# Kernel tuning notes

Hardware: AMD Instinct MI355X
Metric: run time of the kernel (lower is better)

The kernel has to match this reference:

```python
import jax, jax.numpy as jnp
import numpy as np

B, S, D, H = 2, 2048, 1024, 16
DH = D // H  # 64
EPS = 1e-5


def setup_inputs() -> dict:
    key = jax.random.key(0)
    ks = jax.random.split(key, 16)
    s = 0.02
    return {
        "emb": jax.random.normal(ks[0], (B, S, D), dtype=jnp.float32),
        # per-head projections, stacked: torch Linear weight layout [out, in] -> [H, DH, D]
        "Wq": jax.random.normal(ks[1], (H, DH, D), dtype=jnp.float32) * s,
        "bq": jnp.zeros((H, DH), dtype=jnp.float32),
        "Wk": jax.random.normal(ks[2], (H, DH, D), dtype=jnp.float32) * s,
        "bk": jnp.zeros((H, DH), dtype=jnp.float32),
        "Wv": jax.random.normal(ks[3], (H, DH, D), dtype=jnp.float32) * s,
        "bv": jnp.zeros((H, DH), dtype=jnp.float32),
        "W0": jax.random.normal(ks[4], (D, D), dtype=jnp.float32) * s,
        "b0": jnp.zeros((D,), dtype=jnp.float32),
        "g1": jnp.ones((D,), dtype=jnp.float32),
        "be1": jnp.zeros((D,), dtype=jnp.float32),
        "W1": jax.random.normal(ks[5], (4 * D, D), dtype=jnp.float32) * s,
        "b1": jnp.zeros((4 * D,), dtype=jnp.float32),
        "W2": jax.random.normal(ks[6], (D, 4 * D), dtype=jnp.float32) * s,
        "b2": jnp.zeros((D,), dtype=jnp.float32),
        "g2": jnp.ones((D,), dtype=jnp.float32),
        "be2": jnp.zeros((D,), dtype=jnp.float32),
    }


def _layer_norm(x, g, b):
    mu = jnp.mean(x, axis=-1, keepdims=True)
    var = jnp.mean(jnp.square(x - mu), axis=-1, keepdims=True)
    return (x - mu) * jax.lax.rsqrt(var + EPS) * g + b


def reference(emb, Wq, bq, Wk, bk, Wv, bv, W0, b0, g1, be1, W1, b1, W2, b2, g2, be2):
    # per-head Q/K/V projections, batched over heads  -> [B, H, S, DH]
    q = jnp.einsum("bsd,hed->bhse", emb, Wq) + bq[None, :, None, :]
    k = jnp.einsum("bsd,hed->bhse", emb, Wk) + bk[None, :, None, :]
    v = jnp.einsum("bsd,hed->bhse", emb, Wv) + bv[None, :, None, :]
    # NOTE: original module applies NO scale before softmax; it divides the
    # softmax(QK^T) @ V output by sqrt(d_head) afterwards. Kept faithfully.
    scores = jnp.einsum("bhse,bhte->bhst", q, k)  # [B,H,S,S]
    attn = jax.nn.softmax(scores, axis=-1)
    z = jnp.einsum("bhst,bhte->bhse", attn, v) / np.sqrt(DH).astype(np.float32)
    # concat heads along feature dim (head 0 first) -> [B, S, D]
    z = z.transpose(0, 2, 1, 3).reshape(B, S, D)
    z = z @ W0.T + b0
    out1 = _layer_norm(z + emb, g1, be1)
    h = jax.nn.relu(out1 @ W1.T + b1)  # [B, S, 4D]
    out2 = _layer_norm(out1 + (h @ W2.T + b2), g2, be2)
    return out2
```

## Files before the change

### kernel.cpp

```cpp
#include <hip/hip_runtime.h>
#include <hip/hip_bf16.h>
#include <cstdint>
#include <cmath>

#define DEV __device__ __forceinline__

typedef float f32x4 __attribute__((ext_vector_type(4)));
typedef float f32x16 __attribute__((ext_vector_type(16)));
typedef __bf16 bf16x8 __attribute__((ext_vector_type(8)));
typedef unsigned short u16;
typedef u16 u16x8 __attribute__((ext_vector_type(8)));
typedef u16 u16x4 __attribute__((ext_vector_type(4)));

DEV u16 f2bf(float f) {
  union { float f; uint32_t u; } x{f};
  uint32_t r = x.u + 0x7FFFu + ((x.u >> 16) & 1u);
  return (u16)(r >> 16);
}

DEV void gl_lds16(const u16* g, u16* l) {
  __builtin_amdgcn_global_load_lds((const __attribute__((address_space(1))) void*)g,
                                   (__attribute__((address_space(3))) void*)l, 16, 0, 0);
}

__global__ __launch_bounds__(256) void k_cvt(const float* __restrict__ s,
                                             u16* __restrict__ d, int n) {
  int step = gridDim.x * blockDim.x * 4;
  for (int i = (blockIdx.x * blockDim.x + threadIdx.x) * 4; i < n; i += step) {
    float4 v = *reinterpret_cast<const float4*>(s + i);
    u16x4 o;
    o[0] = f2bf(v.x); o[1] = f2bf(v.y); o[2] = f2bf(v.z); o[3] = f2bf(v.w);
    *reinterpret_cast<u16x4*>(d + i) = o;
  }
}

__global__ __launch_bounds__(256) void k_cvt4(
    const float* __restrict__ s0, const float* __restrict__ s1,
    const float* __restrict__ s2, const float* __restrict__ s3,
    u16* __restrict__ d0, u16* __restrict__ d1,
    u16* __restrict__ d2, u16* __restrict__ d3, int n) {
  const int y = blockIdx.y;
  const float* s = (y == 0) ? s0 : (y == 1) ? s1 : (y == 2) ? s2 : s3;
  u16* d = (y == 0) ? d0 : (y == 1) ? d1 : (y == 2) ? d2 : d3;
  int step = gridDim.x * blockDim.x * 4;
  for (int i = (blockIdx.x * blockDim.x + threadIdx.x) * 4; i < n; i += step) {
    float4 v = *reinterpret_cast<const float4*>(s + i);
    u16x4 o;
    o[0] = f2bf(v.x); o[1] = f2bf(v.y); o[2] = f2bf(v.z); o[3] = f2bf(v.w);
    *reinterpret_cast<u16x4*>(d + i) = o;
  }
}


template <int MODE>
DEV void gemm_core128(const u16* __restrict__ A, const u16* __restrict__ B,
                      const float* __restrict__ bias, const float* __restrict__ res,
                      void* __restrict__ C, int N, int K, int m0, int n0,
                      float oscale) {
  __shared__ u16 sA[2][128 * 32];
  __shared__ u16 sB[2][128 * 32];
  const int tid = threadIdx.x;
  const int w = tid >> 6, l = tid & 63;
  const int lr = l & 15, lg = l >> 4;
  const int wr = (w >> 1) * 64, wc = (w & 1) * 64;

  f32x4 acc[4][4] = {};

  const int nt = K >> 5;
  const int sr = w * 16 + (l >> 2);
  const int sc = (l & 3) * 8;

  auto stage = [&](int buf, int t) {
    const u16* ga = A + (size_t)(m0 + sr) * K + t * 32 + sc;
    const u16* gb = B + (size_t)(n0 + sr) * K + t * 32 + sc;
    gl_lds16(ga, &sA[buf][w * 512]);
    gl_lds16(ga + (size_t)64 * K, &sA[buf][2048 + w * 512]);
    gl_lds16(gb, &sB[buf][w * 512]);
    gl_lds16(gb + (size_t)64 * K, &sB[buf][2048 + w * 512]);
  };

  auto compute = [&](int buf) {
    bf16x8 af[4], bfr[4];
#pragma unroll
    for (int mf = 0; mf < 4; ++mf)
      af[mf] = *(const bf16x8*)&sA[buf][(wr + mf * 16 + lr) * 32 + lg * 8];
#pragma unroll
    for (int nf = 0; nf < 4; ++nf)
      bfr[nf] = *(const bf16x8*)&sB[buf][(wc + nf * 16 + lr) * 32 + lg * 8];
#pragma unroll
    for (int mf = 0; mf < 4; ++mf)
#pragma unroll
      for (int nf = 0; nf < 4; ++nf)
        acc[mf][nf] = __builtin_amdgcn_mfma_f32_16x16x32_bf16(af[mf], bfr[nf],
                                                              acc[mf][nf], 0, 0, 0);
  };

  stage(0, 0);
  __syncthreads();
  int cur = 0;
  for (int t = 0; t < nt - 1; ++t) {
    stage(cur ^ 1, t + 1);
    compute(cur);
    __syncthreads();
    cur ^= 1;
  }
  compute(cur);

#pragma unroll
  for (int nf = 0; nf < 4; ++nf) {
    const int col = n0 + wc + nf * 16 + lr;
    const float bv = bias[col];
#pragma unroll
    for (int mf = 0; mf < 4; ++mf) {
      const int row0 = m0 + wr + mf * 16 + lg * 4;
#pragma unroll
      for (int r = 0; r < 4; ++r) {
        float v = acc[mf][nf][r] + bv;
        if (MODE == 0) v *= oscale;
        if (MODE == 1) v = fmaxf(v, 0.0f);
        const size_t idx = (size_t)(row0 + r) * N + col;
        if (MODE == 2) ((float*)C)[idx] = v + res[idx];
        else ((u16*)C)[idx] = f2bf(v);
      }
    }
  }
}

template <int MODE>
DEV void gemm_core64(const u16* __restrict__ A, const u16* __restrict__ B,
                     const float* __restrict__ bias, const float* __restrict__ res,
                     void* __restrict__ C, int N, int K, int m0, int n0,
                     float oscale) {
  __shared__ u16 sA[2][64 * 32];
  __shared__ u16 sB[2][128 * 32];
  const int tid = threadIdx.x;
  const int w = tid >> 6, l = tid & 63;
  const int lr = l & 15, lg = l >> 4;
  const int wr = (w >> 1) * 32, wc = (w & 1) * 64;

  f32x4 acc[2][4] = {};

  const int nt = K >> 5;
  const int sr = w * 16 + (l >> 2);
  const int sc = (l & 3) * 8;

  auto stage = [&](int buf, int t) {
    gl_lds16(A + (size_t)(m0 + sr) * K + t * 32 + sc, &sA[buf][w * 512]);
    const u16* gb = B + (size_t)(n0 + sr) * K + t * 32 + sc;
    gl_lds16(gb, &sB[buf][w * 512]);
    gl_lds16(gb + (size_t)64 * K, &sB[buf][2048 + w * 512]);
  };

  auto compute = [&](int buf) {
    bf16x8 af[2], bfr[4];
#pragma unroll
    for (int mf = 0; mf < 2; ++mf)
      af[mf] = *(const bf16x8*)&sA[buf][(wr + mf * 16 + lr) * 32 + lg * 8];
#pragma unroll
    for (int nf = 0; nf < 4; ++nf)
      bfr[nf] = *(const bf16x8*)&sB[buf][(wc + nf * 16 + lr) * 32 + lg * 8];
#pragma unroll
    for (int mf = 0; mf < 2; ++mf)
#pragma unroll
      for (int nf = 0; nf < 4; ++nf)
        acc[mf][nf] = __builtin_amdgcn_mfma_f32_16x16x32_bf16(af[mf], bfr[nf],
                                                              acc[mf][nf], 0, 0, 0);
  };

  stage(0, 0);
  __syncthreads();
  int cur = 0;
  for (int t = 0; t < nt - 1; ++t) {
    stage(cur ^ 1, t + 1);
    compute(cur);
    __syncthreads();
    cur ^= 1;
  }
  compute(cur);

#pragma unroll
  for (int nf = 0; nf < 4; ++nf) {
    const int col = n0 + wc + nf * 16 + lr;
    const float bv = bias[col];
#pragma unroll
    for (int mf = 0; mf < 2; ++mf) {
      const int row0 = m0 + wr + mf * 16 + lg * 4;
#pragma unroll
      for (int r = 0; r < 4; ++r) {
        float v = acc[mf][nf][r] + bv;
        if (MODE == 0) v *= oscale;
        if (MODE == 1) v = fmaxf(v, 0.0f);
        const size_t idx = (size_t)(row0 + r) * N + col;
        if (MODE == 2) ((float*)C)[idx] = v + res[idx];
        else ((u16*)C)[idx] = f2bf(v);
      }
    }
  }
}

template <int MODE>
__global__ __launch_bounds__(256) void k_gemm(const u16* __restrict__ A,
                                              const u16* __restrict__ B,
                                              const float* __restrict__ bias,
                                              const float* __restrict__ res,
                                              void* __restrict__ C, int N, int K) {
  gemm_core128<MODE>(A, B, bias, res, C, N, K, blockIdx.x * 128, blockIdx.y * 128, 1.0f);
}

template <int MODE>
__global__ __launch_bounds__(256) void k_gemm64(const u16* __restrict__ A,
                                                const u16* __restrict__ B,
                                                const float* __restrict__ bias,
                                                const float* __restrict__ res,
                                                void* __restrict__ C, int N, int K) {
  gemm_core64<MODE>(A, B, bias, res, C, N, K, blockIdx.x * 64, blockIdx.y * 128, 1.0f);
}

__global__ __launch_bounds__(256) void k_gemm_qkv(
    const u16* __restrict__ A, const u16* __restrict__ B0, const u16* __restrict__ B1,
    const u16* __restrict__ B2, const float* __restrict__ c0,
    const float* __restrict__ c1, const float* __restrict__ c2,
    u16* __restrict__ O0, u16* __restrict__ O1, u16* __restrict__ O2) {
  const int z = blockIdx.z;
  const u16* B = (z == 0) ? B0 : (z == 1) ? B1 : B2;
  const float* bias = (z == 0) ? c0 : (z == 1) ? c1 : c2;
  u16* O = (z == 0) ? O0 : (z == 1) ? O1 : O2;
  const float sc = (z == 0) ? 1.44269504f : 1.0f;
  gemm_core64<0>(A, B, bias, nullptr, O, 1024, 1024, blockIdx.x * 64,
                 blockIdx.y * 128, sc);
}

__global__ __launch_bounds__(256) void k_attn(const u16* __restrict__ Q,
                                              const u16* __restrict__ K,
                                              const u16* __restrict__ V,
                                              u16* __restrict__ Z) {
  const int id = blockIdx.x;
  const int virt = (id & 7) * 64 + (id >> 3);
  const int bh = virt >> 4;
  const int qt = virt & 15;
  const int b = bh >> 4, h = bh & 15;
  const int tid = threadIdx.x;
  const int w = tid >> 6, l = tid & 63;
  const int q32 = l & 31, hi = l >> 5;

  __shared__ u16 Kl[2][64 * 64];
  __shared__ u16 VT[2][64 * 64];

  const size_t rb = (size_t)b * 2048;
  const int c0 = h * 64;
  const int q0w = qt * 128 + w * 32;

  bf16x8 qb[4];
#pragma unroll
  for (int st = 0; st < 4; ++st)
    qb[st] = *(const bf16x8*)(Q + (rb + q0w + q32) * 1024 + c0 + st * 16 + hi * 8);

  f32x16 zacc[2] = {};
  float mrun = -1e30f, lrun = 0.f;

  const int skv = w * 16 + (l >> 3);
  const int sc8 = l & 7;
  auto stage_k = [&](int pp, int t) {
#pragma unroll
    for (int cq = 0; cq < 2; ++cq) {
      const int kvl = skv + cq * 8;
      const int dh0 = (sc8 ^ (kvl & 7)) * 8;
      gl_lds16(K + (rb + t * 64 + kvl) * 1024 + c0 + dh0,
               &Kl[pp][w * 1024 + cq * 512]);
    }
  };

  const int vp = tid & 31, vd0 = (tid >> 5) * 8;
  u16x8 va0, va1;
  auto vload = [&](int t) {
    const u16* v0 = V + (rb + t * 64 + 2 * vp) * 1024 + c0 + vd0;
    va0 = *(const u16x8*)v0;
    va1 = *(const u16x8*)(v0 + 1024);
  };
  auto vstore = [&](int pp) {
#pragma unroll
    for (int i = 0; i < 8; ++i) {
      const int dh = vd0 + i;
      const int off = ((2 * vp) & 7) + 8 * ((vp >> 2) ^ (dh & 7));
      uint32_t pk = (uint32_t)va0[i] | ((uint32_t)va1[i] << 16);
      *(uint32_t*)&VT[pp][dh * 64 + off] = pk;
    }
  };

  stage_k(0, 0);
  vload(0);
  vstore(0);
  __syncthreads();

  for (int t = 0; t < 32; ++t) {
    const int p = t & 1;
    if (t + 1 < 32) {
      stage_k(p ^ 1, t + 1);
      vload(t + 1);
    }
    f32x16 s[2] = {};
    __builtin_amdgcn_s_setprio(1);
#pragma unroll
    for (int nf = 0; nf < 2; ++nf)
#pragma unroll
      for (int st = 0; st < 4; ++st) {
        bf16x8 ka = *(const bf16x8*)&Kl[p][(nf * 32 + q32) * 64 +
                                           ((st * 2 + hi) ^ (q32 & 7)) * 8];
        s[nf] = __builtin_amdgcn_mfma_f32_32x32x16_bf16(ka, qb[st], s[nf], 0, 0, 0);
      }
    __builtin_amdgcn_s_setprio(0);

    float m = s[0][0];
#pragma unroll
    for (int r = 1; r < 16; ++r) m = fmaxf(m, s[0][r]);
#pragma unroll
    for (int r = 0; r < 16; ++r) m = fmaxf(m, s[1][r]);
    m = fmaxf(m, __shfl_xor(m, 32, 64));

    if (__any(m > mrun + 8.0f)) {
      float mn = fmaxf(mrun, m);
      float sc = exp2f(mrun - mn);
      mrun = mn;
      lrun *= sc;
#pragma unroll
      for (int r = 0; r < 16; ++r) {
        float scr = __shfl(sc, (r & 3) + 8 * (r >> 2) + 4 * hi, 64);
        zacc[0][r] *= scr;
        zacc[1][r] *= scr;
      }
    }

    uint32_t c[16];
#pragma unroll
    for (int nf = 0; nf < 2; ++nf)
#pragma unroll
      for (int m2 = 0; m2 < 8; ++m2) {
        float p0 = exp2f(s[nf][2 * m2] - mrun);
        float p1 = exp2f(s[nf][2 * m2 + 1] - mrun);
        lrun += p0 + p1;
        uint32_t pk;
        asm("v_cvt_pk_bf16_f32 %0, %1, %2" : "=v"(pk) : "v"(p0), "v"(p1));
        c[nf * 8 + m2] = pk;
      }
#pragma unroll
    for (int ks = 0; ks < 4; ++ks) {
      asm("v_permlane32_swap_b32 %0, %1" : "+v"(c[4 * ks]), "+v"(c[4 * ks + 2]));
      asm("v_permlane32_swap_b32 %0, %1" : "+v"(c[4 * ks + 1]), "+v"(c[4 * ks + 3]));
    }

    if (t + 1 < 32) vstore(p ^ 1);

    __builtin_amdgcn_s_setprio(1);
#pragma unroll
    for (int ks = 0; ks < 4; ++ks) {
      union { uint32_t u[4]; bf16x8 v; } pa;
#pragma unroll
      for (int i = 0; i < 4; ++i) pa.u[i] = c[4 * ks + i];
#pragma unroll
      for (int nd = 0; nd < 2; ++nd) {
        bf16x8 vb = *(const bf16x8*)&VT[p][(nd * 32 + q32) * 64 +
                                           ((ks * 2 + hi) ^ (q32 & 7)) * 8];
        zacc[nd] = __builtin_amdgcn_mfma_f32_32x32x16_bf16(pa.v, vb, zacc[nd], 0, 0, 0);
      }
    }
    __builtin_amdgcn_s_setprio(0);
    __syncthreads();
  }

  float ltot = lrun + __shfl_xor(lrun, 32, 64);
  float inv = 0.125f / ltot;
#pragma unroll
  for (int r = 0; r < 16; ++r) {
    float invr = __shfl(inv, (r & 3) + 8 * (r >> 2) + 4 * hi, 64);
    const size_t row = rb + q0w + (r & 3) + 8 * (r >> 2) + 4 * hi;
#pragma unroll
    for (int nd = 0; nd < 2; ++nd)
      Z[row * 1024 + c0 + nd * 32 + q32] = f2bf(zacc[nd][r] * invr);
  }
}

template <bool WBF>
__global__ __launch_bounds__(256) void k_ln(const float* __restrict__ x,
                                            const float* __restrict__ g,
                                            const float* __restrict__ be,
                                            float* __restrict__ of,
                                            u16* __restrict__ ob) {
  const int row = blockIdx.x;
  const int tid = threadIdx.x;
  const float* xr = x + (size_t)row * 1024;
  float4 v = *(const float4*)(xr + tid * 4);
  float s = v.x + v.y + v.z + v.w;
  float s2 = v.x * v.x + v.y * v.y + v.z * v.z + v.w * v.w;
#pragma unroll
  for (int st = 1; st < 64; st <<= 1) {
    s += __shfl_xor(s, st, 64);
    s2 += __shfl_xor(s2, st, 64);
  }
  __shared__ float ps[8];
  if ((tid & 63) == 0) { ps[tid >> 6] = s; ps[4 + (tid >> 6)] = s2; }
  __syncthreads();
  s = ps[0] + ps[1] + ps[2] + ps[3];
  s2 = ps[4] + ps[5] + ps[6] + ps[7];
  const float mu = s * 0.0009765625f;
  const float var = s2 * 0.0009765625f - mu * mu;
  const float rs = rsqrtf(var + 1e-5f);
  float4 gg = *(const float4*)(g + tid * 4);
  float4 bb = *(const float4*)(be + tid * 4);
  float4 o;
  o.x = (v.x - mu) * rs * gg.x + bb.x;
  o.y = (v.y - mu) * rs * gg.y + bb.y;
  o.z = (v.z - mu) * rs * gg.z + bb.z;
  o.w = (v.w - mu) * rs * gg.w + bb.w;
  *(float4*)(of + (size_t)row * 1024 + tid * 4) = o;
  if (WBF) {
    u16x4 q;
    q[0] = f2bf(o.x); q[1] = f2bf(o.y); q[2] = f2bf(o.z); q[3] = f2bf(o.w);
    *(u16x4*)(ob + (size_t)row * 1024 + tid * 4) = q;
  }
}

extern "C" void kernel_launch(void* const* d_in, const int* in_sizes, int n_in,
                              void* d_out, int out_size, void* d_ws, size_t ws_size,
                              hipStream_t stream) {
  const float* emb = (const float*)d_in[0];
  const float* Wq  = (const float*)d_in[1];
  const float* bq  = (const float*)d_in[2];
  const float* Wk  = (const float*)d_in[3];
  const float* bk  = (const float*)d_in[4];
  const float* Wv  = (const float*)d_in[5];
  const float* bv  = (const float*)d_in[6];
  const float* W0  = (const float*)d_in[7];
  const float* b0  = (const float*)d_in[8];
  const float* g1  = (const float*)d_in[9];
  const float* be1 = (const float*)d_in[10];
  const float* W1  = (const float*)d_in[11];
  const float* b1  = (const float*)d_in[12];
  const float* W2  = (const float*)d_in[13];
  const float* b2  = (const float*)d_in[14];
  const float* g2  = (const float*)d_in[15];
  const float* be2 = (const float*)d_in[16];

  char* p = (char*)d_ws;
  auto alloc = [&](size_t bytes) { char* r = p; p += bytes; return r; };
  u16* embb = (u16*)alloc(8u << 20);
  u16* Wqb  = (u16*)alloc(2u << 20);
  u16* Wkb  = (u16*)alloc(2u << 20);
  u16* Wvb  = (u16*)alloc(2u << 20);
  u16* W0b  = (u16*)alloc(2u << 20);
  u16* W1b  = (u16*)alloc(8u << 20);
  u16* W2b  = (u16*)alloc(8u << 20);
  u16* Qb   = (u16*)alloc(8u << 20);
  u16* Kb   = (u16*)alloc(8u << 20);
  u16* Vb   = (u16*)alloc(8u << 20);
  u16* Zb   = (u16*)alloc(8u << 20);
  float* y1 = (float*)alloc(16u << 20);
  float* o1f = (float*)alloc(16u << 20);
  u16* o1b  = (u16*)alloc(8u << 20);
  u16* hb   = (u16*)alloc(32u << 20);

  auto cvt = [&](const float* s, u16* d, int n) {
    int blk = (n / 4 + 255) / 256;
    if (blk > 4096) blk = 4096;
    k_cvt<<<blk, 256, 0, stream>>>(s, d, n);
  };
  cvt(emb, embb, 4096 * 1024);
  k_cvt4<<<dim3(1024, 4), 256, 0, stream>>>(Wq, Wk, Wv, W0, Wqb, Wkb, Wvb, W0b,
                                            1024 * 1024);
  cvt(W1, W1b, 4096 * 1024);
  cvt(W2, W2b, 4096 * 1024);

  k_gemm_qkv<<<dim3(64, 8, 3), 256, 0, stream>>>(embb, Wqb, Wkb, Wvb, bq, bk, bv,
                                                 Qb, Kb, Vb);
  k_attn<<<dim3(512), 256, 0, stream>>>(Qb, Kb, Vb, Zb);
  k_gemm64<2><<<dim3(64, 8), 256, 0, stream>>>(Zb, W0b, b0, emb, y1, 1024, 1024);
  k_ln<true><<<4096, 256, 0, stream>>>(y1, g1, be1, o1f, o1b);
  k_gemm<1><<<dim3(32, 32), 256, 0, stream>>>(o1b, W1b, b1, nullptr, hb, 4096, 1024);
  k_gemm64<2><<<dim3(64, 8), 256, 0, stream>>>(hb, W2b, b2, o1f, y1, 1024, 4096);
  k_ln<false><<<4096, 256, 0, stream>>>(y1, g2, be2, (float*)d_out, nullptr);
}
```

Measured before the change: 312.2 us.

## Split attention KV sequence across two wave teams and merge softmax states

The attention kernel now runs 512 threads per block, as two teams of four waves. Each team processes alternating 64-key tiles with its own double-buffered K/V LDS slices, and the two partial softmax states are merged through shared memory at the end. This doubles the waves working on each query tile, which is meant to hide latency and raise occupancy during the long KV loop, at the cost of more LDS, an extra merge step and a block-wide barrier. Separately, all fp32-to-bf16 weight and input conversions are fused into one launch, and the row-max reduction is rewritten as a tree.

```diff
diff --git a/kernel.cpp b/kernel.cpp
--- a/kernel.cpp
+++ b/kernel.cpp
@@ -23,31 +23,40 @@
                                    (__attribute__((address_space(3))) void*)l, 16, 0, 0);
 }
 
-__global__ __launch_bounds__(256) void k_cvt(const float* __restrict__ s,
-                                             u16* __restrict__ d, int n) {
-  int step = gridDim.x * blockDim.x * 4;
-  for (int i = (blockIdx.x * blockDim.x + threadIdx.x) * 4; i < n; i += step) {
-    float4 v = *reinterpret_cast<const float4*>(s + i);
+DEV float max16(const f32x16& v) {
+  float a = fmaxf(fmaxf(v[0], v[1]), v[2]);
+  float b = fmaxf(fmaxf(v[3], v[4]), v[5]);
+  float c = fmaxf(fmaxf(v[6], v[7]), v[8]);
+  float d = fmaxf(fmaxf(v[9], v[10]), v[11]);
+  float e = fmaxf(fmaxf(v[12], v[13]), v[14]);
+  float x = fmaxf(fmaxf(a, b), c);
+  float y = fmaxf(fmaxf(d, e), v[15]);
+  return fmaxf(x, y);
+}
+
+__global__ __launch_bounds__(256) void k_cvt_all(
+    const float* __restrict__ emb, const float* __restrict__ Wq,
+    const float* __restrict__ Wk, const float* __restrict__ Wv,
+    const float* __restrict__ W0, const float* __restrict__ W1,
+    const float* __restrict__ W2,
+    u16* __restrict__ embb, u16* __restrict__ Wqb, u16* __restrict__ Wkb,
+    u16* __restrict__ Wvb, u16* __restrict__ W0b, u16* __restrict__ W1b,
+    u16* __restrict__ W2b) {
+  const int step = gridDim.x * blockDim.x;
+  for (int i4 = blockIdx.x * blockDim.x + threadIdx.x; i4 < 4194304; i4 += step) {
+    const int i = i4 * 4;
+    const float* s; u16* d; int off;
+    if (i < 4194304)       { s = emb; d = embb; off = 0; }
+    else if (i < 5242880)  { s = Wq;  d = Wqb;  off = 4194304; }
+    else if (i < 6291456)  { s = Wk;  d = Wkb;  off = 5242880; }
+    else if (i < 7340032)  { s = Wv;  d = Wvb;  off = 6291456; }
+    else if (i < 8388608)  { s = W0;  d = W0b;  off = 7340032; }
+    else if (i < 12582912) { s = W1;  d = W1b;  off = 8388608; }
+    else                   { s = W2;  d = W2b;  off = 12582912; }
+    float4 v = *reinterpret_cast<const float4*>(s + (i - off));
     u16x4 o;
     o[0] = f2bf(v.x); o[1] = f2bf(v.y); o[2] = f2bf(v.z); o[3] = f2bf(v.w);
-    *reinterpret_cast<u16x4*>(d + i) = o;
-  }
-}
-
-__global__ __launch_bounds__(256) void k_cvt4(
-    const float* __restrict__ s0, const float* __restrict__ s1,
-    const float* __restrict__ s2, const float* __restrict__ s3,
-    u16* __restrict__ d0, u16* __restrict__ d1,
-    u16* __restrict__ d2, u16* __restrict__ d3, int n) {
-  const int y = blockIdx.y;
-  const float* s = (y == 0) ? s0 : (y == 1) ? s1 : (y == 2) ? s2 : s3;
-  u16* d = (y == 0) ? d0 : (y == 1) ? d1 : (y == 2) ? d2 : d3;
-  int step = gridDim.x * blockDim.x * 4;
-  for (int i = (blockIdx.x * blockDim.x + threadIdx.x) * 4; i < n; i += step) {
-    float4 v = *reinterpret_cast<const float4*>(s + i);
-    u16x4 o;
-    o[0] = f2bf(v.x); o[1] = f2bf(v.y); o[2] = f2bf(v.z); o[3] = f2bf(v.w);
-    *reinterpret_cast<u16x4*>(d + i) = o;
+    *reinterpret_cast<u16x4*>(d + (i - off)) = o;
   }
 }
 
@@ -230,7 +239,7 @@
                  blockIdx.y * 128, sc);
 }
 
-__global__ __launch_bounds__(256) void k_attn(const u16* __restrict__ Q,
+__global__ __launch_bounds__(512) void k_attn(const u16* __restrict__ Q,
                                               const u16* __restrict__ K,
                                               const u16* __restrict__ V,
                                               u16* __restrict__ Z) {
@@ -240,11 +249,15 @@
   const int qt = virt & 15;
   const int b = bh >> 4, h = bh & 15;
   const int tid = threadIdx.x;
-  const int w = tid >> 6, l = tid & 63;
+  const int w8 = tid >> 6;
+  const int team = w8 >> 2;
+  const int w = w8 & 3;
+  const int l = tid & 63;
   const int q32 = l & 31, hi = l >> 5;
 
-  __shared__ u16 Kl[2][64 * 64];
-  __shared__ u16 VT[2][64 * 64];
+  __shared__ u16 Kl[2][2][4096];
+  __shared__ u16 VT[2][2][4096];
+  __shared__ float ML[2][4][64];
 
   const size_t rb = (size_t)b * 2048;
   const int c0 = h * 64;
@@ -260,43 +273,44 @@
 
   const int skv = w * 16 + (l >> 3);
   const int sc8 = l & 7;
-  auto stage_k = [&](int pp, int t) {
+  auto stage_k = [&](int bp, int t) {
 #pragma unroll
     for (int cq = 0; cq < 2; ++cq) {
       const int kvl = skv + cq * 8;
       const int dh0 = (sc8 ^ (kvl & 7)) * 8;
       gl_lds16(K + (rb + t * 64 + kvl) * 1024 + c0 + dh0,
-               &Kl[pp][w * 1024 + cq * 512]);
-    }
-  };
-
-  const int vp = tid & 31, vd0 = (tid >> 5) * 8;
+               &Kl[bp][team][w * 1024 + cq * 512]);
+    }
+  };
+
+  const int ttid = tid & 255;
+  const int vp = ttid & 31, vd0 = (ttid >> 5) * 8;
   u16x8 va0, va1;
   auto vload = [&](int t) {
     const u16* v0 = V + (rb + t * 64 + 2 * vp) * 1024 + c0 + vd0;
     va0 = *(const u16x8*)v0;
     va1 = *(const u16x8*)(v0 + 1024);
   };
-  auto vstore = [&](int pp) {
+  auto vstore = [&](int bp) {
 #pragma unroll
     for (int i = 0; i < 8; ++i) {
       const int dh = vd0 + i;
       const int off = ((2 * vp) & 7) + 8 * ((vp >> 2) ^ (dh & 7));
       uint32_t pk = (uint32_t)va0[i] | ((uint32_t)va1[i] << 16);
-      *(uint32_t*)&VT[pp][dh * 64 + off] = pk;
-    }
-  };
-
-  stage_k(0, 0);
-  vload(0);
+      *(uint32_t*)&VT[bp][team][dh * 64 + off] = pk;
+    }
+  };
+
+  stage_k(0, team);
+  vload(team);
   vstore(0);
   __syncthreads();
 
-  for (int t = 0; t < 32; ++t) {
-    const int p = t & 1;
-    if (t + 1 < 32) {
-      stage_k(p ^ 1, t + 1);
-      vload(t + 1);
+  for (int s2 = 0; s2 < 16; ++s2) {
+    const int bp = s2 & 1;
+    if (s2 + 1 < 16) {
+      stage_k(bp ^ 1, 2 * (s2 + 1) + team);
+      vload(2 * (s2 + 1) + team);
     }
     f32x16 s[2] = {};
     __builtin_amdgcn_s_setprio(1);
@@ -304,17 +318,13 @@
     for (int nf = 0; nf < 2; ++nf)
 #pragma unroll
       for (int st = 0; st < 4; ++st) {
-        bf16x8 ka = *(const bf16x8*)&Kl[p][(nf * 32 + q32) * 64 +
-                                           ((st * 2 + hi) ^ (q32 & 7)) * 8];
+        bf16x8 ka = *(const bf16x8*)&Kl[bp][team][(nf * 32 + q32) * 64 +
+                                                  ((st * 2 + hi) ^ (q32 & 7)) * 8];
         s[nf] = __builtin_amdgcn_mfma_f32_32x32x16_bf16(ka, qb[st], s[nf], 0, 0, 0);
       }
     __builtin_amdgcn_s_setprio(0);
 
-    float m = s[0][0];
-#pragma unroll
-    for (int r = 1; r < 16; ++r) m = fmaxf(m, s[0][r]);
-#pragma unroll
-    for (int r = 0; r < 16; ++r) m = fmaxf(m, s[1][r]);
+    float m = fmaxf(max16(s[0]), max16(s[1]));
     m = fmaxf(m, __shfl_xor(m, 32, 64));
 
     if (__any(m > mrun + 8.0f)) {
@@ -348,7 +358,7 @@
       asm("v_permlane32_swap_b32 %0, %1" : "+v"(c[4 * ks + 1]), "+v"(c[4 * ks + 3]));
     }
 
-    if (t + 1 < 32) vstore(p ^ 1);
+    if (s2 + 1 < 16) vstore(bp ^ 1);
 
     __builtin_amdgcn_s_setprio(1);
 #pragma unroll
@@ -358,8 +368,8 @@
       for (int i = 0; i < 4; ++i) pa.u[i] = c[4 * ks + i];
 #pragma unroll
       for (int nd = 0; nd < 2; ++nd) {
-        bf16x8 vb = *(const bf16x8*)&VT[p][(nd * 32 + q32) * 64 +
-                                           ((ks * 2 + hi) ^ (q32 & 7)) * 8];
+        bf16x8 vb = *(const bf16x8*)&VT[bp][team][(nd * 32 + q32) * 64 +
+                                                  ((ks * 2 + hi) ^ (q32 & 7)) * 8];
         zacc[nd] = __builtin_amdgcn_mfma_f32_32x32x16_bf16(pa.v, vb, zacc[nd], 0, 0, 0);
       }
     }
@@ -367,15 +377,39 @@
     __syncthreads();
   }
 
-  float ltot = lrun + __shfl_xor(lrun, 32, 64);
-  float inv = 0.125f / ltot;
-#pragma unroll
-  for (int r = 0; r < 16; ++r) {
-    float invr = __shfl(inv, (r & 3) + 8 * (r >> 2) + 4 * hi, 64);
-    const size_t row = rb + q0w + (r & 3) + 8 * (r >> 2) + 4 * hi;
+  float* zshare = (float*)&Kl[0][0][0];
+  if (team == 1) {
 #pragma unroll
     for (int nd = 0; nd < 2; ++nd)
-      Z[row * 1024 + c0 + nd * 32 + q32] = f2bf(zacc[nd][r] * invr);
+#pragma unroll
+      for (int r = 0; r < 16; ++r)
+        zshare[(nd * 16 + r) * 256 + w * 64 + l] = zacc[nd][r];
+    ML[0][w][l] = mrun;
+    ML[1][w][l] = lrun;
+  }
+  __syncthreads();
+  if (team == 0) {
+    const float mB = ML[0][w][l];
+    const float lB = ML[1][w][l];
+    const float mM = fmaxf(mrun, mB);
+    const float sA = exp2f(mrun - mM);
+    const float sB = exp2f(mB - mM);
+    const float lh = lrun * sA + lB * sB;
+    const float ltot = lh + __shfl_xor(lh, 32, 64);
+    const float inv = 0.125f / ltot;
+#pragma unroll
+    for (int r = 0; r < 16; ++r) {
+      const int crow = (r & 3) + 8 * (r >> 2) + 4 * hi;
+      const float sAr = __shfl(sA, crow, 64);
+      const float sBr = __shfl(sB, crow, 64);
+      const float invr = __shfl(inv, crow, 64);
+      const size_t row = rb + q0w + crow;
+#pragma unroll
+      for (int nd = 0; nd < 2; ++nd) {
+        float z = zacc[nd][r] * sAr + zshare[(nd * 16 + r) * 256 + w * 64 + l] * sBr;
+        Z[row * 1024 + c0 + nd * 32 + q32] = f2bf(z * invr);
+      }
+    }
   }
 }
 
@@ -458,20 +492,12 @@
   u16* o1b  = (u16*)alloc(8u << 20);
   u16* hb   = (u16*)alloc(32u << 20);
 
-  auto cvt = [&](const float* s, u16* d, int n) {
-    int blk = (n / 4 + 255) / 256;
-    if (blk > 4096) blk = 4096;
-    k_cvt<<<blk, 256, 0, stream>>>(s, d, n);
-  };
-  cvt(emb, embb, 4096 * 1024);
-  k_cvt4<<<dim3(1024, 4), 256, 0, stream>>>(Wq, Wk, Wv, W0, Wqb, Wkb, Wvb, W0b,
-                                            1024 * 1024);
-  cvt(W1, W1b, 4096 * 1024);
-  cvt(W2, W2b, 4096 * 1024);
+  k_cvt_all<<<2048, 256, 0, stream>>>(emb, Wq, Wk, Wv, W0, W1, W2,
+                                      embb, Wqb, Wkb, Wvb, W0b, W1b, W2b);
 
   k_gemm_qkv<<<dim3(64, 8, 3), 256, 0, stream>>>(embb, Wqb, Wkb, Wvb, bq, bk, bv,
                                                  Qb, Kb, Vb);
-  k_attn<<<dim3(512), 256, 0, stream>>>(Qb, Kb, Vb, Zb);
+  k_attn<<<dim3(512), 512, 0, stream>>>(Qb, Kb, Vb, Zb);
   k_gemm64<2><<<dim3(64, 8), 256, 0, stream>>>(Zb, W0b, b0, emb, y1, 1024, 1024);
   k_ln<true><<<4096, 256, 0, stream>>>(y1, g1, be1, o1f, o1b);
   k_gemm<1><<<dim3(32, 32), 256, 0, stream>>>(o1b, W1b, b1, nullptr, hb, 4096, 1024);
```

New measurement: 317.4 us. Within noise of the previous version (+1.7%).
